# Kernel tuning notes

Hardware: AMD Instinct MI355X
Metric: run time of the kernel (lower is better)

The kernel has to match this reference:

```python
import jax, jax.numpy as jnp
import numpy as np

NEG_INF = -1.0e9  # matches the module's explicit -1e9 masking constant


def setup_inputs() -> dict:
    key = jax.random.key(0)
    B, T, D = 8, 2048, 1024
    x = jax.random.normal(key, (B, T, D), dtype=jnp.float32)
    return {"x": x}


def reference(x):
    # x: [B, T, D]
    T = x.shape[1]
    # raw QK^T scores: [B, T, T]
    scores = jnp.einsum('btd,bsd->bts', x, x)
    # torch.tril(scores, -1) + torch.triu(ones*-1e9, 0):
    # keep strictly-lower entries, set diagonal and upper to -1e9.
    strict_lower = jnp.tril(jnp.ones((T, T), dtype=bool), k=-1)
    scores = jnp.where(strict_lower, scores, jnp.float32(NEG_INF))
    # NOTE: row 0 is all -1e9 -> softmax yields uniform 1/T (faithful to the torch code).
    att_weights = jax.nn.softmax(scores, axis=-1)  # [B, T, T]
    att_vec = jnp.einsum('bts,bsd->btd', att_weights, x)  # [B, T, D]
    return att_vec, att_weights
```

## Files before the change

### kernel.cpp

```cpp
#include <hip/hip_runtime.h>

#define B_ 8
#define T_ 2048
#define D_ 1024

typedef __attribute__((ext_vector_type(8))) short bf16x8;
typedef __attribute__((ext_vector_type(8))) _Float16 f16x8;
typedef __attribute__((ext_vector_type(4))) float f32x4;
typedef __attribute__((ext_vector_type(8))) unsigned short u16x8;
typedef __attribute__((ext_vector_type(4))) unsigned short u16x4;

__device__ __forceinline__ unsigned short f2bf(float f) {
  union { float f; unsigned u; } v; v.f = f;
  unsigned r = v.u + 0x7FFFu + ((v.u >> 16) & 1u);
  return (unsigned short)(r >> 16);
}
__device__ __forceinline__ float bf2f(unsigned short h) {
  union { unsigned u; float f; } v; v.u = ((unsigned)h) << 16; return v.f;
}
__device__ __forceinline__ unsigned short f2h(float f) {
  union { _Float16 h; unsigned short u; } v; v.h = (_Float16)f; return v.u;
}
__device__ __forceinline__ float h2f(unsigned short u) {
  union { unsigned short u; _Float16 h; } v; v.u = u; return (float)v.h;
}

__device__ __forceinline__ void gl2lds16(const void* g, void* l) {
  __builtin_amdgcn_global_load_lds(
      (__attribute__((address_space(1))) void*)g,
      (__attribute__((address_space(3))) void*)l, 16, 0, 0);
}

__global__ __launch_bounds__(256) void prep_kernel(
    const float* __restrict__ x,
    unsigned short* __restrict__ xh, unsigned short* __restrict__ xl,
    unsigned short* __restrict__ xth, float* __restrict__ part) {
  const int b = blockIdx.z;
  const int t0 = blockIdx.y << 6;
  const int d0 = blockIdx.x << 6;
  __shared__ unsigned short tf[64][68];
  const int tid = threadIdx.x;
  const int r = tid >> 2, cq = tid & 3;
  const size_t xoff = ((size_t)b * T_ + t0 + r) * D_ + d0;
#pragma unroll
  for (int k = 0; k < 4; ++k) {
    const int col = (cq << 2) + (k << 4);
    const float4 v = *(const float4*)(x + xoff + col);
    const unsigned short h0 = f2bf(v.x), h1 = f2bf(v.y), h2 = f2bf(v.z), h3 = f2bf(v.w);
    const unsigned short l0 = f2bf(v.x - bf2f(h0)), l1 = f2bf(v.y - bf2f(h1));
    const unsigned short l2 = f2bf(v.z - bf2f(h2)), l3 = f2bf(v.w - bf2f(h3));
    u16x4 hv = {h0, h1, h2, h3}, lv = {l0, l1, l2, l3};
    *(u16x4*)(xh + xoff + col) = hv;
    *(u16x4*)(xl + xoff + col) = lv;
    tf[col + 0][r] = f2h(v.x); tf[col + 1][r] = f2h(v.y);
    tf[col + 2][r] = f2h(v.z); tf[col + 3][r] = f2h(v.w);
  }
  __syncthreads();
  const int dr = tid >> 2, tq = tid & 3;
  const size_t toff = ((size_t)b * D_ + d0 + dr) * T_ + t0;
  float cs = 0.f;
#pragma unroll
  for (int c = 0; c < 2; ++c) {
    const int tcol = (tq << 3) + (c << 5);
    const u16x8 vv = *(const u16x8*)&tf[dr][tcol];
    *(u16x8*)(xth + toff + tcol) = vv;
#pragma unroll
    for (int e = 0; e < 8; ++e) cs += h2f(vv[e]);
  }
  cs += __shfl_xor(cs, 1);
  cs += __shfl_xor(cs, 2);
  if (tq == 0)
    part[(((size_t)b << 5) + blockIdx.y) * D_ + d0 + dr] = cs;
}

__global__ __launch_bounds__(256, 4) void scores_mfma(
    const unsigned short* __restrict__ xh, const unsigned short* __restrict__ xl,
    float* __restrict__ w) {
  const int id = blockIdx.x;
  const int sid = ((id & 7) * 136) + (id >> 3);
  const int b = sid / 136;
  const int L = sid - b * 136;
  int tt = (int)((sqrtf(8.f * (float)L + 1.f) - 1.f) * 0.5f);
  while (((tt + 1) * (tt + 2) >> 1) <= L) ++tt;
  while (((tt * (tt + 1)) >> 1) > L) --tt;
  const int ts = L - ((tt * (tt + 1)) >> 1);

  const int t0 = tt << 7, s0 = ts << 7;
  __shared__ unsigned short Ah[128 * 32];
  __shared__ unsigned short Al[128 * 32];
  __shared__ unsigned short Bh[128 * 32];
  __shared__ unsigned short Bl[128 * 32];
  const int tid = threadIdx.x;
  const int lane = tid & 63, wv = tid >> 6;
  const int wr = (wv >> 1) << 6, wc = (wv & 1) << 6;
  const int quad = lane >> 4, r16 = lane & 15;
  const int swz = ((quad ^ (r16 & 3) ^ ((r16 >> 2) & 1)) << 3);
  const size_t xb = (size_t)b * T_ * D_;

  f32x4 acc[4][4];
#pragma unroll
  for (int i = 0; i < 4; ++i)
#pragma unroll
    for (int j = 0; j < 4; ++j) acc[i][j] = (f32x4){0.f, 0.f, 0.f, 0.f};

  for (int k0 = 0; k0 < D_; k0 += 32) {
    __syncthreads();
#pragma unroll
    for (int i = 0; i < 2; ++i) {
      const int cc = (wv << 7) + (i << 6) + lane;
      const int row = cc >> 2, q = cc & 3;
      const int gq = q ^ (row & 3) ^ ((row >> 2) & 1);
      const int ldsoff = (((wv << 7) + (i << 6)) << 3);
      const size_t ga = xb + (size_t)(t0 + row) * D_ + k0 + (gq << 3);
      const size_t gb = xb + (size_t)(s0 + row) * D_ + k0 + (gq << 3);
      gl2lds16(xh + ga, &Ah[ldsoff]);
      gl2lds16(xl + ga, &Al[ldsoff]);
      gl2lds16(xh + gb, &Bh[ldsoff]);
      gl2lds16(xl + gb, &Bl[ldsoff]);
    }
    __syncthreads();
    bf16x8 ah[4], al[4];
#pragma unroll
    for (int i = 0; i < 4; ++i) {
      const int ra = ((wr + (i << 4) + r16) << 5) + swz;
      ah[i] = *(const bf16x8*)&Ah[ra];
      al[i] = *(const bf16x8*)&Al[ra];
    }
#pragma unroll
    for (int j = 0; j < 4; ++j) {
      const int rb = ((wc + (j << 4) + r16) << 5) + swz;
      const bf16x8 bhj = *(const bf16x8*)&Bh[rb];
      const bf16x8 blj = *(const bf16x8*)&Bl[rb];
#pragma unroll
      for (int i = 0; i < 4; ++i)
        acc[i][j] = __builtin_amdgcn_mfma_f32_16x16x32_bf16(ah[i], bhj, acc[i][j], 0, 0, 0);
#pragma unroll
      for (int i = 0; i < 4; ++i)
        acc[i][j] = __builtin_amdgcn_mfma_f32_16x16x32_bf16(ah[i], blj, acc[i][j], 0, 0, 0);
#pragma unroll
      for (int i = 0; i < 4; ++i)
        acc[i][j] = __builtin_amdgcn_mfma_f32_16x16x32_bf16(al[i], bhj, acc[i][j], 0, 0, 0);
    }
  }

  float* wb = w + (size_t)b * T_ * T_;
#pragma unroll
  for (int i = 0; i < 4; ++i)
#pragma unroll
    for (int j = 0; j < 4; ++j) {
      const int rr = t0 + wr + (i << 4) + (quad << 2);
      const int cc = s0 + wc + (j << 4) + r16;
#pragma unroll
      for (int rg = 0; rg < 4; ++rg)
        wb[(size_t)(rr + rg) * T_ + cc] = acc[i][j][rg];
    }
}

template <bool EMIT>
__global__ __launch_bounds__(256) void softmax_kernel(float* __restrict__ w,
                                                      unsigned short* __restrict__ wf) {
  const int row = (blockIdx.x << 2) + (threadIdx.x >> 6);
  const int t = row & (T_ - 1);
  const int lane = threadIdx.x & 63;
  float* wr = w + (size_t)row * T_;
  unsigned short* wfr = wf + (size_t)row * T_;

  if (t == 0) {
    const float u = 1.0f / 2048.0f;
    const f32x4 uv = {u, u, u, u};
#pragma unroll
    for (int k = 0; k < 8; ++k)
      __builtin_nontemporal_store(uv, (f32x4*)&wr[(lane << 2) + (k << 8)]);
    if (EMIT && lane < 32) {
      u16x4 z = {0, 0, 0, 0};
      *(u16x4*)&wfr[lane << 2] = z;
    }
    return;
  }

  float4 v[8];
  float m = -3.0e38f;
#pragma unroll
  for (int k = 0; k < 8; ++k) {
    const int s = (lane << 2) + (k << 8);
    float4 val = {-1.0e30f, -1.0e30f, -1.0e30f, -1.0e30f};
    if (s < t) {
      const float4 g = *(const float4*)&wr[s];
      val.x = g.x;
      val.y = (s + 1 < t) ? g.y : -1.0e30f;
      val.z = (s + 2 < t) ? g.z : -1.0e30f;
      val.w = (s + 3 < t) ? g.w : -1.0e30f;
    }
    v[k] = val;
    m = fmaxf(m, fmaxf(fmaxf(val.x, val.y), fmaxf(val.z, val.w)));
  }
#pragma unroll
  for (int off = 32; off; off >>= 1) m = fmaxf(m, __shfl_xor(m, off));

  float l = 0.f;
#pragma unroll
  for (int k = 0; k < 8; ++k) {
    v[k].x = __expf(v[k].x - m);
    v[k].y = __expf(v[k].y - m);
    v[k].z = __expf(v[k].z - m);
    v[k].w = __expf(v[k].w - m);
    l += (v[k].x + v[k].y) + (v[k].z + v[k].w);
  }
#pragma unroll
  for (int off = 32; off; off >>= 1) l += __shfl_xor(l, off);
  const float inv = 1.0f / l;

  const int smax_emit = ((t >> 7) + 1) << 7;
#pragma unroll
  for (int k = 0; k < 8; ++k) {
    const int s = (lane << 2) + (k << 8);
    const f32x4 o = {v[k].x * inv, v[k].y * inv, v[k].z * inv, v[k].w * inv};
    __builtin_nontemporal_store(o, (f32x4*)&wr[s]);
    if (EMIT && s < smax_emit) {
      u16x4 h = {f2h(o[0]), f2h(o[1]), f2h(o[2]), f2h(o[3])};
      *(u16x4*)&wfr[s] = h;
    }
  }
}

template <bool USE_WF16>
__global__ __launch_bounds__(256, 4) void av_mfma(
    const float* __restrict__ w, const unsigned short* __restrict__ wf,
    const unsigned short* __restrict__ xth, float* __restrict__ out) {
  const int xid = blockIdx.x;
  const int td = xid >> 3;
  const int kp = xid & 7;
  const int b = blockIdx.z;
  const int d0 = td << 7;
  __shared__ unsigned short Aw[128 * 64];
  __shared__ unsigned short Bx[128 * 64];
  const int tid = threadIdx.x;
  const int lane = tid & 63, wv = tid >> 6;
  const int wr = (wv >> 1) << 6, wc = (wv & 1) << 6;
  const int quad = lane >> 4, r16 = lane & 15;
  const size_t xtb = (size_t)b * D_ * T_;
  const size_t wbase = (size_t)b * T_ * T_;
  float* ob = out + (size_t)b * T_ * D_;

#pragma unroll 1
  for (int mtile = 0; mtile < 2; ++mtile) {
    const int tt = mtile ? (15 - kp) : kp;
    const int t0 = tt << 7;
    const int smax = t0 + 128;

    f32x4 acc[4][4];
#pragma unroll
    for (int i = 0; i < 4; ++i)
#pragma unroll
      for (int j = 0; j < 4; ++j) acc[i][j] = (f32x4){0.f, 0.f, 0.f, 0.f};

    for (int s0 = 0; s0 < smax; s0 += 64) {
      __syncthreads();
      if (USE_WF16) {
#pragma unroll
        for (int i = 0; i < 4; ++i) {
          const int cc = (wv << 8) + (i << 6) + lane;
          const int rowa = cc >> 3, q = cc & 7;
          const int gq = q ^ (rowa & 7);
          const int ldsoff = (((wv << 8) + (i << 6)) << 3);
          gl2lds16(wf + wbase + (size_t)(t0 + rowa) * T_ + s0 + (gq << 3), &Aw[ldsoff]);
        }
      } else {
        const int rowa = tid >> 1, half = tid & 1;
        const float* g = w + wbase + (size_t)(t0 + rowa) * T_ + s0 + (half << 5);
        const int rs = rowa & 7;
#pragma unroll
        for (int p = 0; p < 4; ++p) {
          const float4 va = ((const float4*)g)[2 * p];
          const float4 vb = ((const float4*)g)[2 * p + 1];
          u16x8 pk = {f2h(va.x), f2h(va.y), f2h(va.z), f2h(va.w),
                      f2h(vb.x), f2h(vb.y), f2h(vb.z), f2h(vb.w)};
          const int c = (half << 2) + p;
          *(u16x8*)&Aw[(rowa << 6) + ((c ^ rs) << 3)] = pk;
        }
      }
#pragma unroll
      for (int i = 0; i < 4; ++i) {
        const int cc = (wv << 8) + (i << 6) + lane;
        const int rowb = cc >> 3, q = cc & 7;
        const int gq = q ^ (rowb & 7);
        const int ldsoff = (((wv << 8) + (i << 6)) << 3);
        gl2lds16(xth + xtb + (size_t)(d0 + rowb) * T_ + s0 + (gq << 3), &Bx[ldsoff]);
      }
      __syncthreads();
#pragma unroll
      for (int h = 0; h < 2; ++h) {
        f16x8 a[4];
#pragma unroll
        for (int i = 0; i < 4; ++i) {
          const int ar = wr + (i << 4) + r16;
          a[i] = *(const f16x8*)&Aw[(ar << 6) + ((((h << 2) | quad) ^ (ar & 7)) << 3)];
        }
#pragma unroll
        for (int j = 0; j < 4; ++j) {
          const int br = wc + (j << 4) + r16;
          const f16x8 bbj = *(const f16x8*)&Bx[(br << 6) + ((((h << 2) | quad) ^ (br & 7)) << 3)];
#pragma unroll
          for (int i = 0; i < 4; ++i)
            acc[i][j] = __builtin_amdgcn_mfma_f32_16x16x32_f16(a[i], bbj, acc[i][j], 0, 0, 0);
        }
      }
    }

#pragma unroll
    for (int i = 0; i < 4; ++i)
#pragma unroll
      for (int j = 0; j < 4; ++j) {
        const int rr = t0 + wr + (i << 4) + (quad << 2);
        const int cc = d0 + wc + (j << 4) + r16;
#pragma unroll
        for (int rg = 0; rg < 4; ++rg)
          __builtin_nontemporal_store(acc[i][j][rg], &ob[(size_t)(rr + rg) * D_ + cc]);
      }
  }
}

__global__ __launch_bounds__(256) void row0_reduce(const float* __restrict__ part,
                                                   float* __restrict__ out) {
  const int b = blockIdx.x;
  const int tid = threadIdx.x;
  float4 s = {0.f, 0.f, 0.f, 0.f};
#pragma unroll 8
  for (int p = 0; p < 32; ++p) {
    const float4 v = *(const float4*)(part + (((size_t)b << 5) + p) * D_ + (tid << 2));
    s.x += v.x; s.y += v.y; s.z += v.z; s.w += v.w;
  }
  const float sc = 1.0f / 2048.0f;
  float4 o = {s.x * sc, s.y * sc, s.z * sc, s.w * sc};
  *(float4*)(out + (size_t)b * T_ * D_ + (tid << 2)) = o;
}

extern "C" void kernel_launch(void* const* d_in, const int* in_sizes, int n_in,
                              void* d_out, int out_size, void* d_ws, size_t ws_size,
                              hipStream_t stream) {
  const float* x = (const float*)d_in[0];
  float* att_vec = (float*)d_out;
  float* w = (float*)d_out + (size_t)B_ * T_ * D_;

  unsigned short* xh = (unsigned short*)att_vec;
  unsigned short* xl = xh + (size_t)B_ * T_ * D_;
  const size_t xthN = (size_t)B_ * D_ * T_;
  const size_t wfN = (size_t)B_ * T_ * T_;
  unsigned short* xth = (unsigned short*)d_ws;
  unsigned short* wf16 = xth + xthN;
  const size_t need = xthN * 2 + wfN * 2 + (size_t)256 * D_ * 4;
  const bool use_wf16 = (ws_size >= need);
  float* part = use_wf16 ? (float*)(wf16 + wfN) : (float*)(xth + xthN);

  prep_kernel<<<dim3(D_ / 64, T_ / 64, B_), 256, 0, stream>>>(x, xh, xl, xth, part);
  scores_mfma<<<dim3(8 * 136), 256, 0, stream>>>(xh, xl, w);
  if (use_wf16) {
    softmax_kernel<true><<<dim3(B_ * T_ / 4), 256, 0, stream>>>(w, wf16);
    av_mfma<true><<<dim3(64, 1, B_), 256, 0, stream>>>(w, wf16, xth, att_vec);
  } else {
    softmax_kernel<false><<<dim3(B_ * T_ / 4), 256, 0, stream>>>(w, wf16);
    av_mfma<false><<<dim3(64, 1, B_), 256, 0, stream>>>(w, wf16, xth, att_vec);
  }
  row0_reduce<<<dim3(B_), 256, 0, stream>>>(part, att_vec);
}
```

Before: 468.6 us.

## Double-buffer LDS tiles in scores MFMA kernel to overlap loads with compute

The scores GEMM kernel now keeps two LDS buffers per operand and issues the global-to-LDS loads for the next K step before computing on the current one. Explicit vmcnt waits and raw s_barrier calls replace the two __syncthreads per iteration. The goal is to hide global load latency behind MFMA work. LDS use doubles and the launch-bounds occupancy hint drops from 4 to 2 blocks, so fewer waves are resident to hide latency.

```diff
diff --git a/kernel.cpp b/kernel.cpp
--- a/kernel.cpp
+++ b/kernel.cpp
@@ -73,7 +73,7 @@
     part[(((size_t)b << 5) + blockIdx.y) * D_ + d0 + dr] = cs;
 }
 
-__global__ __launch_bounds__(256, 4) void scores_mfma(
+__global__ __launch_bounds__(256, 2) void scores_mfma(
     const unsigned short* __restrict__ xh, const unsigned short* __restrict__ xl,
     float* __restrict__ w) {
   const int id = blockIdx.x;
@@ -86,10 +86,10 @@
   const int ts = L - ((tt * (tt + 1)) >> 1);
 
   const int t0 = tt << 7, s0 = ts << 7;
-  __shared__ unsigned short Ah[128 * 32];
-  __shared__ unsigned short Al[128 * 32];
-  __shared__ unsigned short Bh[128 * 32];
-  __shared__ unsigned short Bl[128 * 32];
+  __shared__ unsigned short Ah[2][128 * 32];
+  __shared__ unsigned short Al[2][128 * 32];
+  __shared__ unsigned short Bh[2][128 * 32];
+  __shared__ unsigned short Bl[2][128 * 32];
   const int tid = threadIdx.x;
   const int lane = tid & 63, wv = tid >> 6;
   const int wr = (wv >> 1) << 6, wc = (wv & 1) << 6;
@@ -97,40 +97,63 @@
   const int swz = ((quad ^ (r16 & 3) ^ ((r16 >> 2) & 1)) << 3);
   const size_t xb = (size_t)b * T_ * D_;
 
+  const int cc0 = (wv << 7) + lane;
+  const int cc1 = cc0 + 64;
+  const int row0 = cc0 >> 2, q0 = cc0 & 3;
+  const int row1 = cc1 >> 2, q1 = cc1 & 3;
+  const int gq0 = q0 ^ (row0 & 3) ^ ((row0 >> 2) & 1);
+  const int gq1 = q1 ^ (row1 & 3) ^ ((row1 >> 2) & 1);
+  const int lo0 = ((wv << 7) << 3);
+  const int lo1 = (((wv << 7) + 64) << 3);
+
   f32x4 acc[4][4];
 #pragma unroll
   for (int i = 0; i < 4; ++i)
 #pragma unroll
     for (int j = 0; j < 4; ++j) acc[i][j] = (f32x4){0.f, 0.f, 0.f, 0.f};
 
-  for (int k0 = 0; k0 < D_; k0 += 32) {
-    __syncthreads();
-#pragma unroll
-    for (int i = 0; i < 2; ++i) {
-      const int cc = (wv << 7) + (i << 6) + lane;
-      const int row = cc >> 2, q = cc & 3;
-      const int gq = q ^ (row & 3) ^ ((row >> 2) & 1);
-      const int ldsoff = (((wv << 7) + (i << 6)) << 3);
-      const size_t ga = xb + (size_t)(t0 + row) * D_ + k0 + (gq << 3);
-      const size_t gb = xb + (size_t)(s0 + row) * D_ + k0 + (gq << 3);
-      gl2lds16(xh + ga, &Ah[ldsoff]);
-      gl2lds16(xl + ga, &Al[ldsoff]);
-      gl2lds16(xh + gb, &Bh[ldsoff]);
-      gl2lds16(xl + gb, &Bl[ldsoff]);
-    }
-    __syncthreads();
+#define SCORES_STAGE(nb, k0)                                                   \
+  {                                                                            \
+    const size_t ga0 = xb + (size_t)(t0 + row0) * D_ + (k0) + (gq0 << 3);      \
+    const size_t gb0 = xb + (size_t)(s0 + row0) * D_ + (k0) + (gq0 << 3);      \
+    const size_t ga1 = xb + (size_t)(t0 + row1) * D_ + (k0) + (gq1 << 3);      \
+    const size_t gb1 = xb + (size_t)(s0 + row1) * D_ + (k0) + (gq1 << 3);      \
+    gl2lds16(xh + ga0, &Ah[nb][lo0]);                                          \
+    gl2lds16(xl + ga0, &Al[nb][lo0]);                                          \
+    gl2lds16(xh + gb0, &Bh[nb][lo0]);                                          \
+    gl2lds16(xl + gb0, &Bl[nb][lo0]);                                          \
+    gl2lds16(xh + ga1, &Ah[nb][lo1]);                                          \
+    gl2lds16(xl + ga1, &Al[nb][lo1]);                                          \
+    gl2lds16(xh + gb1, &Bh[nb][lo1]);                                          \
+    gl2lds16(xl + gb1, &Bl[nb][lo1]);                                          \
+  }
+
+  SCORES_STAGE(0, 0)
+
+  for (int step = 0; step < 32; ++step) {
+    const int cur = step & 1;
+    __builtin_amdgcn_s_barrier();
+    if (step + 1 < 32) {
+      SCORES_STAGE(cur ^ 1, (step + 1) << 5)
+      asm volatile("s_waitcnt vmcnt(8)" ::: "memory");
+    } else {
+      asm volatile("s_waitcnt vmcnt(0)" ::: "memory");
+    }
+    __builtin_amdgcn_sched_barrier(0);
+    __builtin_amdgcn_s_barrier();
+
     bf16x8 ah[4], al[4];
 #pragma unroll
     for (int i = 0; i < 4; ++i) {
       const int ra = ((wr + (i << 4) + r16) << 5) + swz;
-      ah[i] = *(const bf16x8*)&Ah[ra];
-      al[i] = *(const bf16x8*)&Al[ra];
+      ah[i] = *(const bf16x8*)&Ah[cur][ra];
+      al[i] = *(const bf16x8*)&Al[cur][ra];
     }
 #pragma unroll
     for (int j = 0; j < 4; ++j) {
       const int rb = ((wc + (j << 4) + r16) << 5) + swz;
-      const bf16x8 bhj = *(const bf16x8*)&Bh[rb];
-      const bf16x8 blj = *(const bf16x8*)&Bl[rb];
+      const bf16x8 bhj = *(const bf16x8*)&Bh[cur][rb];
+      const bf16x8 blj = *(const bf16x8*)&Bl[cur][rb];
 #pragma unroll
       for (int i = 0; i < 4; ++i)
         acc[i][j] = __builtin_amdgcn_mfma_f32_16x16x32_bf16(ah[i], bhj, acc[i][j], 0, 0, 0);
@@ -142,6 +165,7 @@
         acc[i][j] = __builtin_amdgcn_mfma_f32_16x16x32_bf16(al[i], bhj, acc[i][j], 0, 0, 0);
     }
   }
+#undef SCORES_STAGE
 
   float* wb = w + (size_t)b * T_ * T_;
 #pragma unroll
```

Measured after the change: 464.2 us. About the same (-0.9%).
